# Kernel optimization log

Measured on AMD Instinct MI355X. Metric: run time of the kernel, lower is better.

The kernel has to match this reference:

```python
import jax, jax.numpy as jnp
import numpy as np

N_SRC = 100000
N_TGT = 100000
N_EDGES = 1600000
D = 128
HID = 128
OUT = 64
NUM_LAYERS = 2
P_DROP = 0.1
NEG_SLOPE = 0.01


def setup_inputs() -> dict:
    key = jax.random.key(0)
    ks = jax.random.split(key, 16)
    s = 1.0 / np.sqrt(D)
    inp = {
        "x_source": jax.random.normal(ks[0], (N_SRC, D), jnp.float32),
        "x_target": jax.random.normal(ks[1], (N_TGT, D), jnp.float32),
        "Wl_tgt": jax.random.normal(ks[2], (NUM_LAYERS, D, HID), jnp.float32) * s,
        "bl_tgt": jax.random.normal(ks[3], (NUM_LAYERS, HID), jnp.float32) * s,
        "Wr_tgt": jax.random.normal(ks[4], (NUM_LAYERS, D, HID), jnp.float32) * s,
        "Wl_src": jax.random.normal(ks[5], (NUM_LAYERS, D, HID), jnp.float32) * s,
        "bl_src": jax.random.normal(ks[6], (NUM_LAYERS, HID), jnp.float32) * s,
        "Wr_src": jax.random.normal(ks[7], (NUM_LAYERS, D, HID), jnp.float32) * s,
        "W_out": jax.random.normal(ks[8], (HID, OUT), jnp.float32) * (1.0 / np.sqrt(HID)),
        "b_out": jax.random.normal(ks[9], (OUT,), jnp.float32) * 0.01,
        "edge_src": jax.random.randint(ks[10], (N_EDGES,), 0, N_SRC, jnp.int32),
        "edge_dst": jax.random.randint(ks[11], (N_EDGES,), 0, N_TGT, jnp.int32),
        "rev_src": jax.random.randint(ks[12], (N_EDGES,), 0, N_TGT, jnp.int32),
        "rev_dst": jax.random.randint(ks[13], (N_EDGES,), 0, N_SRC, jnp.int32),
    }
    return inp


def _sage(x_src, x_dst, src_idx, dst_idx, n_dst, Wl, bl, Wr):
    # mean-aggregate neighbor messages per destination node (PyG SAGEConv default)
    msg = x_src[src_idx]  # [E, D] gather
    agg = jax.ops.segment_sum(msg, dst_idx, num_segments=n_dst)  # [n_dst, D]
    cnt = jax.ops.segment_sum(jnp.ones((src_idx.shape[0],), msg.dtype), dst_idx,
                              num_segments=n_dst)
    mean = agg / jnp.maximum(cnt, 1.0)[:, None]
    return mean @ Wl + bl + x_dst @ Wr


def _dropout(x, key):
    keep = jax.random.bernoulli(key, 1.0 - P_DROP, x.shape)
    return jnp.where(keep, x / (1.0 - P_DROP), jnp.zeros((), x.dtype))


def reference(x_source, x_target, Wl_tgt, bl_tgt, Wr_tgt, Wl_src, bl_src, Wr_src,
              W_out, b_out, edge_src, edge_dst, rev_src, rev_dst):
    dkey = jax.random.key(42)
    xs, xt = x_source, x_target
    for l in range(NUM_LAYERS):
        # ('source','edge','target'): target receives from source
        new_t = _sage(xs, xt, edge_src, edge_dst, N_TGT, Wl_tgt[l], bl_tgt[l], Wr_tgt[l])
        # ('target','rev_edge','source'): source receives from target
        new_s = _sage(xt, xs, rev_src, rev_dst, N_SRC, Wl_src[l], bl_src[l], Wr_src[l])
        new_t = jax.nn.leaky_relu(new_t, NEG_SLOPE)
        new_s = jax.nn.leaky_relu(new_s, NEG_SLOPE)
        new_t = _dropout(new_t, jax.random.fold_in(dkey, 2 * l))
        new_s = _dropout(new_s, jax.random.fold_in(dkey, 2 * l + 1))
        xs, xt = new_s, new_t
    return xs @ W_out + b_out
```

## Files before the change

### kernel.cpp

```cpp
#include <hip/hip_runtime.h>
#include <stdint.h>

#define NN 100000
#define NE 1600000
#define DD 128
#define HB 1024
#define G8 12544
#define SUBN 98
#define NSUB 128
#define NND 100352
#define K2 16
#define RCAP 2304
#define MSKB 1563

typedef unsigned short u16;
typedef unsigned long long u64;
typedef short short8 __attribute__((ext_vector_type(8)));
typedef float floatx4 __attribute__((ext_vector_type(4)));
typedef float floatx2 __attribute__((ext_vector_type(2)));
typedef int intx4 __attribute__((ext_vector_type(4)));

__device__ static inline u16 f2bf(float f){
  unsigned u = __float_as_uint(f);
  unsigned r = u + 0x7FFFu + ((u >> 16) & 1u);
  return (u16)(r >> 16);
}

__host__ __device__ static inline unsigned rotl32(unsigned x, int r){
  return (x << r) | (x >> (32 - r));
}

__host__ __device__ static inline void tf2x32(unsigned k0, unsigned k1,
                                              unsigned c0, unsigned c1,
                                              unsigned &o0, unsigned &o1)
{
  const unsigned ks2 = k0 ^ k1 ^ 0x1BD11BDAu;
  unsigned x0 = c0 + k0, x1 = c1 + k1;
#define TFR(r) { x0 += x1; x1 = rotl32(x1, (r)); x1 ^= x0; }
  TFR(13) TFR(15) TFR(26) TFR(6)   x0 += k1;  x1 += ks2 + 1u;
  TFR(17) TFR(29) TFR(16) TFR(24)  x0 += ks2; x1 += k0 + 2u;
  TFR(13) TFR(15) TFR(26) TFR(6)   x0 += k0;  x1 += k1 + 3u;
  TFR(17) TFR(29) TFR(16) TFR(24)  x0 += k1;  x1 += ks2 + 4u;
  TFR(13) TFR(15) TFR(26) TFR(6)   x0 += ks2; x1 += k0 + 5u;
#undef TFR
  o0 = x0; o1 = x1;
}

__device__ static inline int drop_keep(unsigned k0, unsigned k1, unsigned j)
{
  unsigned o0, o1;
  tf2x32(k0, k1, 0u, j, o0, o1);
  const unsigned bits = o0 ^ o1;
  const float u = __uint_as_float((bits >> 9) | 0x3F800000u) - 1.0f;
  return u < 0.9f;
}

__device__ static inline void mask_body(u64* __restrict__ mp,
                                        unsigned kk0, unsigned kk1, int mb){
  const int wave = threadIdx.x >> 6, lane = threadIdx.x & 63;
  const int base = mb * 64 + wave * 16;
  for (int i2 = 0; i2 < 16; ++i2){
    int r = base + i2;
    if (r >= NN) break;
    u64 mA = __ballot(drop_keep(kk0, kk1, (unsigned)r * 128u + (unsigned)lane));
    u64 mB = __ballot(drop_keep(kk0, kk1, (unsigned)r * 128u + 64u + (unsigned)lane));
    if (lane < 2) mp[(size_t)r * 2 + lane] = lane ? mB : mA;
  }
}

#define CVB 12500
__global__ __launch_bounds__(256) void k_pre(
    const float* __restrict__ ina, const float* __restrict__ inb,
    u16* __restrict__ oa, u16* __restrict__ ob, int n8,
    const int* __restrict__ e_dst, const int* __restrict__ r_dst,
    int* __restrict__ hist,
    const float* __restrict__ Wl_tgt, const float* __restrict__ Wr_tgt,
    const float* __restrict__ Wl_src, const float* __restrict__ Wr_src,
    const float* __restrict__ Wo,
    u16* __restrict__ Wsw0, u16* __restrict__ Wsw1, u16* __restrict__ Wsw2,
    u16* __restrict__ Wswo)
{
  const int blk = blockIdx.x;
  const int t = threadIdx.x;
  if (blk < CVB){
    int i = blk * 256 + t;
    const float* in = ina; u16* out = oa;
    if (i >= n8){ i -= n8; in = inb; out = ob; }
    floatx4 a = __builtin_nontemporal_load((const floatx4*)in + (size_t)i * 2);
    floatx4 c = __builtin_nontemporal_load((const floatx4*)in + (size_t)i * 2 + 1);
    u16 v[8] = { f2bf(a[0]), f2bf(a[1]), f2bf(a[2]), f2bf(a[3]),
                 f2bf(c[0]), f2bf(c[1]), f2bf(c[2]), f2bf(c[3]) };
    *(uint4*)(out + (size_t)i * 8) = *(const uint4*)v;
  } else if (blk < CVB + HB){
    const int hb = blk - CVB;
    __shared__ int h[16];
    if (t < 16) h[t] = 0;
    __syncthreads();
    const int QT = 2 * (NE / 4);
    for (int i = hb * 256 + t; i < QT; i += HB * 256){
      int dir = (i >= NE / 4);
      int qi = dir ? i - NE / 4 : i;
      const int* dp = dir ? r_dst : e_dst;
      intx4 d = __builtin_nontemporal_load((const intx4*)dp + qi);
      int bb = dir << 3;
      atomicAdd(&h[bb + d.x / G8], 1);
      atomicAdd(&h[bb + d.y / G8], 1);
      atomicAdd(&h[bb + d.z / G8], 1);
      atomicAdd(&h[bb + d.w / G8], 1);
    }
    __syncthreads();
    if (t < 16) hist[t * HB + hb] = h[t];
  } else {
    int b = blk - CVB - HB;
    if (b < 48){
      const float *Wl, *Wr; u16* dst;
      if (b < 16){ Wl = Wl_tgt; Wr = Wr_tgt; dst = Wsw0; }
      else if (b < 32){ Wl = Wl_src; Wr = Wr_src; dst = Wsw1; b -= 16; }
      else { Wl = Wl_src + 16384; Wr = Wr_src + 16384; dst = Wsw2; b -= 32; }
      int idx = b * 256 + t;
      int lane = idx & 63, tile = idx >> 6;
      int kt = tile >> 3, nt = tile & 7;
      int n = nt * 16 + (lane & 15);
      int kb = kt * 32 + (lane >> 4) * 8;
      u16 v[8];
      #pragma unroll
      for (int j = 0; j < 8; ++j){
        int k = kb + j;
        float w = (k < 128) ? Wl[(size_t)k * 128 + n] : Wr[(size_t)(k - 128) * 128 + n];
        v[j] = f2bf(w);
      }
      *(uint4*)(dst + (size_t)idx * 8) = *(const uint4*)v;
    } else {
      int idx = (b - 48) * 256 + t;
      int lane = idx & 63, tile = idx >> 6;
      int kt = tile >> 2, nt = tile & 3;
      int n = nt * 16 + (lane & 15);
      int kb = kt * 32 + (lane >> 4) * 8;
      u16 v[8];
      #pragma unroll
      for (int j = 0; j < 8; ++j)
        v[j] = f2bf(Wo[(size_t)(kb + j) * 64 + n]);
      *(uint4*)(Wswo + (size_t)idx * 8) = *(const uint4*)v;
    }
  }
}

__global__ __launch_bounds__(256) void k_scanA(int* __restrict__ hist){
  __shared__ int sh[16 * HB];
  __shared__ int tot[256];
  const int t = threadIdx.x;
  const int N = 16 * HB;
  for (int k = t; k < N; k += 256) sh[k] = hist[k];
  __syncthreads();
  int s = 0;
  #pragma unroll 4
  for (int k = 0; k < 64; ++k)
    s += sh[(t >> 4) * HB + (t & 15) + (k << 4)];
  tot[t] = s;
  __syncthreads();
  int v = s;
  for (int off = 1; off < 256; off <<= 1){
    int u = (t >= off) ? tot[t - off] : 0;
    __syncthreads();
    tot[t] += u;
    __syncthreads();
  }
  int run = tot[t] - v;
  for (int k = 0; k < 64; ++k){
    int idx = (t >> 4) * HB + (t & 15) + (k << 4);
    int xv = sh[idx];
    sh[idx] = run;
    run += xv;
  }
  __syncthreads();
  for (int k = t; k < N; k += 256) hist[k] = sh[k];
  if (t == 255) hist[N] = tot[255];
}

__global__ __launch_bounds__(256) void k_scatter1(const int* __restrict__ e_src,
                                                  const int* __restrict__ e_dst,
                                                  const int* __restrict__ r_src,
                                                  const int* __restrict__ r_dst,
                                                  const int* __restrict__ base,
                                                  unsigned* __restrict__ stage,
                                                  u64* __restrict__ M0t,
                                                  unsigned ka, unsigned kb){
  const int b = blockIdx.x;
  const int q = b / 5, rm = b % 5;
  if (rm >= 2){
    int mb = q * 3 + (rm - 2);
    if (mb < MSKB) mask_body(M0t, ka, kb, mb);
    return;
  }
  const int sb = q * 2 + rm;
  if (sb >= HB) return;
  __shared__ int cur[16];
  const int t = threadIdx.x;
  if (t < 16) cur[t] = base[t * HB + sb];
  __syncthreads();
  const int QT = 2 * (NE / 4);
  for (int i = sb * 256 + t; i < QT; i += HB * 256){
    int dir = (i >= NE / 4);
    int qi = dir ? i - NE / 4 : i;
    const int* dp = dir ? r_dst : e_dst;
    const int* sp = dir ? r_src : e_src;
    intx4 d = __builtin_nontemporal_load((const intx4*)dp + qi);
    intx4 sv = __builtin_nontemporal_load((const intx4*)sp + qi);
    int bb = dir << 3;
    int g, p;
    g = d.x / G8; p = atomicAdd(&cur[bb + g], 1);
    stage[p] = (unsigned)sv.x | ((unsigned)(d.x - g * G8) << 17);
    g = d.y / G8; p = atomicAdd(&cur[bb + g], 1);
    stage[p] = (unsigned)sv.y | ((unsigned)(d.y - g * G8) << 17);
    g = d.z / G8; p = atomicAdd(&cur[bb + g], 1);
    stage[p] = (unsigned)sv.z | ((unsigned)(d.z - g * G8) << 17);
    g = d.w / G8; p = atomicAdd(&cur[bb + g], 1);
    stage[p] = (unsigned)sv.w | ((unsigned)(d.w - g * G8) << 17);
  }
}

__global__ __launch_bounds__(256) void k_hist2(const unsigned* __restrict__ stage,
                                               const int* __restrict__ base,
                                               int* __restrict__ hist2){
  __shared__ int h2[NSUB];
  const int b16 = blockIdx.x / K2, k = blockIdx.x % K2;
  const int t = threadIdx.x;
  if (t < NSUB) h2[t] = 0;
  __syncthreads();
  const int beg = base[b16 * HB];
  const int end = base[(b16 + 1) * HB];
  for (int i = beg + k * 256 + t; i < end; i += K2 * 256){
    unsigned p = stage[i];
    atomicAdd(&h2[(int)(p >> 17) / SUBN], 1);
  }
  __syncthreads();
  if (t < NSUB) hist2[(b16 * NSUB + t) * K2 + k] = h2[t];
}

__global__ __launch_bounds__(256) void k_scanB(int* __restrict__ hist2){
  __shared__ int sh[16 * NSUB * K2];
  __shared__ int tot[256];
  const int t = threadIdx.x;
  const int N = 16 * NSUB * K2;
  for (int k = t; k < N; k += 256) sh[k] = hist2[k];
  __syncthreads();
  int s = 0;
  for (int j = 0; j < 128; ++j) s += sh[t * 128 + j];
  tot[t] = s;
  __syncthreads();
  int v = s;
  for (int off = 1; off < 256; off <<= 1){
    int u = (t >= off) ? tot[t - off] : 0;
    __syncthreads();
    tot[t] += u;
    __syncthreads();
  }
  int run = tot[t] - v;
  for (int j = 0; j < 128; ++j){
    int xv = sh[t * 128 + j];
    sh[t * 128 + j] = run;
    run += xv;
  }
  __syncthreads();
  for (int k = t; k < N; k += 256) hist2[k] = sh[k];
}

__global__ __launch_bounds__(256) void k_scatter2(const unsigned* __restrict__ stage,
                                                  const int* __restrict__ base,
                                                  const int* __restrict__ h2s,
                                                  unsigned* __restrict__ stage2,
                                                  u64* __restrict__ M0s,
                                                  unsigned ka, unsigned kb){
  const int b = blockIdx.x;
  const int q = b / 7, rm = b % 7;
  if (rm >= 1){
    int mb = q * 6 + (rm - 1);
    if (mb < MSKB) mask_body(M0s, ka, kb, mb);
    return;
  }
  const int sb = q;
  if (sb >= 16 * K2) return;
  __shared__ int cur[NSUB];
  const int b16 = sb / K2, k = sb % K2;
  const int t = threadIdx.x;
  if (t < NSUB) cur[t] = h2s[(b16 * NSUB + t) * K2 + k];
  __syncthreads();
  const int beg = base[b16 * HB];
  const int end = base[(b16 + 1) * HB];
  for (int i = beg + k * 256 + t; i < end; i += K2 * 256){
    unsigned p = stage[i];
    int pos = atomicAdd(&cur[(int)(p >> 17) / SUBN], 1);
    stage2[pos] = p;
  }
}

__global__ __launch_bounds__(256) void k_fill4(const unsigned* __restrict__ stage2,
                                               const int* __restrict__ h2s,
                                               int* __restrict__ ptr,
                                               int* __restrict__ csr){
  __shared__ unsigned rec[RCAP];
  __shared__ unsigned srt[RCAP];
  __shared__ int ldeg[SUBN], lptr[SUBN], lcur[SUBN];
  const int sb = blockIdx.x;
  const int b16 = sb >> 7, sub = sb & 127;
  const int dir = b16 >> 3, g = b16 & 7;
  const int t = threadIdx.x;
  const int beg = h2s[sb * K2];
  const int end = (sb == 2047) ? 2 * NE : h2s[(sb + 1) * K2];
  int n = end - beg;
  if (n > RCAP) n = RCAP;
  for (int i = t; i < n; i += 256) rec[i] = stage2[beg + i];
  if (t < SUBN) ldeg[t] = 0;
  __syncthreads();
  const int nl0 = sub * SUBN;
  for (int i = t; i < n; i += 256)
    atomicAdd(&ldeg[(int)(rec[i] >> 17) - nl0], 1);
  __syncthreads();
  if (t == 0){
    int run = 0;
    for (int s = 0; s < SUBN; ++s){ lptr[s] = run; lcur[s] = run; run += ldeg[s]; }
  }
  __syncthreads();
  for (int i = t; i < n; i += 256){
    int rl = (int)(rec[i] >> 17) - nl0;
    int pos = atomicAdd(&lcur[rl], 1);
    srt[pos] = rec[i] & 0x1FFFFu;
  }
  __syncthreads();
  const int node0 = g * G8 + nl0;
  if (t < SUBN) ptr[dir * NND + node0 + t] = beg + lptr[t];
  if (sb == 2047 && t == 0) ptr[2 * NND] = 2 * NE;
  for (int i = t; i < n; i += 256) csr[beg + i] = (int)srt[i];
}

template<bool WM>
__device__ static inline void agg_body(const u16* __restrict__ x,
                                       const int* __restrict__ pd,
                                       const int* __restrict__ csr,
                                       u16* __restrict__ out,
                                       u64* __restrict__ msk,
                                       unsigned key0, unsigned key1, int blk){
  const int row = blk * 4 + (threadIdx.x >> 6);
  const int lane = threadIdx.x & 63;
  const int sub = lane >> 4, l4 = lane & 15;
  const int beg = pd[row], end = pd[row + 1];
  const int cnt = end - beg;
  floatx2 p0 = (floatx2)0.f, p1 = (floatx2)0.f, p2 = (floatx2)0.f, p3 = (floatx2)0.f;
#define ACC4(v) { \
    floatx2 t0, t1, t2, t3; \
    t0[0] = __uint_as_float((v).x << 16); t0[1] = __uint_as_float((v).x & 0xFFFF0000u); \
    t1[0] = __uint_as_float((v).y << 16); t1[1] = __uint_as_float((v).y & 0xFFFF0000u); \
    t2[0] = __uint_as_float((v).z << 16); t2[1] = __uint_as_float((v).z & 0xFFFF0000u); \
    t3[0] = __uint_as_float((v).w << 16); t3[1] = __uint_as_float((v).w & 0xFFFF0000u); \
    p0 += t0; p1 += t1; p2 += t2; p3 += t3; }
  int e = 0;
  for (; e + 7 < cnt; e += 8){
    int s0 = csr[beg + e + sub];
    int s1 = csr[beg + e + 4 + sub];
    uint4 v0 = *(const uint4*)(x + (size_t)s0 * DD + l4 * 8);
    uint4 v1 = *(const uint4*)(x + (size_t)s1 * DD + l4 * 8);
    ACC4(v0);
    ACC4(v1);
  }
  for (; e + 3 < cnt; e += 4){
    int s0 = csr[beg + e + sub];
    uint4 v0 = *(const uint4*)(x + (size_t)s0 * DD + l4 * 8);
    ACC4(v0);
  }
  if (e + sub < cnt){
    int s0 = csr[beg + e + sub];
    uint4 v0 = *(const uint4*)(x + (size_t)s0 * DD + l4 * 8);
    ACC4(v0);
  }
#undef ACC4
  if (WM){
    u64 mA = __ballot(drop_keep(key0, key1, (unsigned)row * 128u + (unsigned)lane));
    u64 mB = __ballot(drop_keep(key0, key1, (unsigned)row * 128u + 64u + (unsigned)lane));
    if (lane < 2) msk[(size_t)row * 2 + lane] = lane ? mB : mA;
  }
  float a[8] = { p0[0], p0[1], p1[0], p1[1], p2[0], p2[1], p3[0], p3[1] };
  #pragma unroll
  for (int i = 0; i < 8; ++i){
    a[i] += __shfl_xor(a[i], 16);
    a[i] += __shfl_xor(a[i], 32);
  }
  const float inv = (cnt > 0) ? (1.0f / (float)cnt) : 1.0f;
  if (sub == 0){
    unsigned pk[4];
    #pragma unroll
    for (int i = 0; i < 4; ++i)
      pk[i] = (unsigned)f2bf(a[2*i] * inv) | ((unsigned)f2bf(a[2*i+1] * inv) << 16);
    *(uint4*)(out + (size_t)row * DD + l4 * 8) = make_uint4(pk[0], pk[1], pk[2], pk[3]);
  }
}

__global__ __launch_bounds__(256) void k_aggD(const u16* __restrict__ x0,
    const u16* __restrict__ x1, const int* __restrict__ ptr,
    const int* __restrict__ csr, u16* __restrict__ o0, u16* __restrict__ o1){
  int b = blockIdx.x;
  if (b < NN / 4) agg_body<false>(x0, ptr, csr, o0, nullptr, 0u, 0u, b);
  else            agg_body<false>(x1, ptr + NND, csr, o1, nullptr, 0u, 0u, b - NN / 4);
}

__global__ __launch_bounds__(256) void k_agg1(const u16* __restrict__ x,
    const int* __restrict__ ptr, const int* __restrict__ csr,
    u16* __restrict__ out, u64* __restrict__ msk,
    unsigned key0, unsigned key1){
  agg_body<true>(x, ptr + NND, csr, out, msk, key0, key1, blockIdx.x);
}

__device__ static inline void fused_body(const u16* __restrict__ Am,
    const u16* __restrict__ X, const u16* __restrict__ Wsw,
    const float* __restrict__ bias, u16* __restrict__ outH,
    const u64* __restrict__ msk, int blk)
{
  const int wave = threadIdx.x >> 6, lane = threadIdx.x & 63;
  const int quad = lane >> 4, col0 = lane & 15;
  const int row0 = blk * 64 + wave * 16;
  int m = row0 + col0;
  if (m >= NN) m = NN - 1;

  floatx4 acc[8];
  #pragma unroll
  for (int i = 0; i < 8; ++i) acc[i] = (floatx4)0.f;

  #pragma unroll
  for (int kt = 0; kt < 8; ++kt){
    const int k = kt * 32 + quad * 8;
    const u16* ap = (k < 128) ? (Am + (size_t)m * 128 + k)
                              : (X  + (size_t)m * 128 + (k - 128));
    short8 a = __builtin_nontemporal_load((const short8*)ap);
    #pragma unroll
    for (int nt = 0; nt < 8; ++nt){
      short8 b = *(const short8*)(Wsw + (size_t)(((kt * 8 + nt) * 64 + lane) * 8));
      acc[nt] = __builtin_amdgcn_mfma_f32_16x16x32_bf16(a, b, acc[nt], 0, 0, 0);
    }
  }

  u64 w0[4], w1[4];
  #pragma unroll
  for (int rg = 0; rg < 4; ++rg){
    int r = row0 + quad * 4 + rg;
    size_t rr = (size_t)((r < NN) ? r : (NN - 1)) * 2;
    w0[rg] = msk[rr];
    w1[rg] = msk[rr + 1];
  }

  #pragma unroll
  for (int nt = 0; nt < 8; ++nt){
    const int col = nt * 16 + col0;
    const float bj = bias[col];
    const int sh = col & 63;
    #pragma unroll
    for (int rg = 0; rg < 4; ++rg){
      const int r = row0 + quad * 4 + rg;
      if (r < NN){
        float h = acc[nt][rg] + bj;
        h = (h >= 0.f) ? h : 0.01f * h;
        u64 w = (nt < 4) ? w0[rg] : w1[rg];
        h = ((w >> sh) & 1ull) ? h * (1.0f / 0.9f) : 0.0f;
        outH[(size_t)r * 128 + col] = f2bf(h);
      }
    }
  }
}

#define GB ((NN + 63) / 64)

__global__ __launch_bounds__(256) void k_fusedD(
    const u16* __restrict__ A0, const u16* __restrict__ X0,
    const u16* __restrict__ W0, const float* __restrict__ b0,
    u16* __restrict__ o0, const u64* __restrict__ m0,
    const u16* __restrict__ A1, const u16* __restrict__ X1,
    const u16* __restrict__ W1, const float* __restrict__ b1,
    u16* __restrict__ o1, const u64* __restrict__ m1)
{
  int b = blockIdx.x;
  if (b < GB) fused_body(A0, X0, W0, b0, o0, m0, b);
  else        fused_body(A1, X1, W1, b1, o1, m1, b - GB);
}

__global__ __launch_bounds__(256) void k_fused(const u16* __restrict__ Am,
    const u16* __restrict__ X, const u16* __restrict__ Wsw,
    const float* __restrict__ bias, u16* __restrict__ outH,
    const u64* __restrict__ msk)
{
  fused_body(Am, X, Wsw, bias, outH, msk, blockIdx.x);
}

__global__ __launch_bounds__(256) void k_out(const u16* __restrict__ H,
    const u16* __restrict__ Wsw, const float* __restrict__ bias,
    float* __restrict__ out)
{
  const int wave = threadIdx.x >> 6, lane = threadIdx.x & 63;
  const int quad = lane >> 4, col0 = lane & 15;
  const int row0 = blockIdx.x * 64 + wave * 16;
  int m = row0 + col0;
  if (m >= NN) m = NN - 1;

  floatx4 acc[4];
  #pragma unroll
  for (int i = 0; i < 4; ++i) acc[i] = (floatx4)0.f;

  #pragma unroll
  for (int kt = 0; kt < 4; ++kt){
    short8 a = __builtin_nontemporal_load(
        (const short8*)(H + (size_t)m * 128 + kt * 32 + quad * 8));
    #pragma unroll
    for (int nt = 0; nt < 4; ++nt){
      short8 b = *(const short8*)(Wsw + (size_t)(((kt * 4 + nt) * 64 + lane) * 8));
      acc[nt] = __builtin_amdgcn_mfma_f32_16x16x32_bf16(a, b, acc[nt], 0, 0, 0);
    }
  }

  #pragma unroll
  for (int nt = 0; nt < 4; ++nt){
    const int col = nt * 16 + col0;
    const float bj = bias[col];
    #pragma unroll
    for (int rg = 0; rg < 4; ++rg){
      const int r = row0 + quad * 4 + rg;
      if (r < NN)
        out[(size_t)r * 64 + col] = acc[nt][rg] + bj;
    }
  }
}

extern "C" void kernel_launch(void* const* d_in, const int* in_sizes, int n_in,
                              void* d_out, int out_size, void* d_ws, size_t ws_size,
                              hipStream_t stream)
{
  const float* x_src  = (const float*)d_in[0];
  const float* x_tgt  = (const float*)d_in[1];
  const float* Wl_tgt = (const float*)d_in[2];
  const float* bl_tgt = (const float*)d_in[3];
  const float* Wr_tgt = (const float*)d_in[4];
  const float* Wl_src = (const float*)d_in[5];
  const float* bl_src = (const float*)d_in[6];
  const float* Wr_src = (const float*)d_in[7];
  const float* W_o    = (const float*)d_in[8];
  const float* b_o    = (const float*)d_in[9];
  const int*   e_src  = (const int*)d_in[10];
  const int*   e_dst  = (const int*)d_in[11];
  const int*   r_src  = (const int*)d_in[12];
  const int*   r_dst  = (const int*)d_in[13];
  float* out = (float*)d_out;
  (void)in_sizes; (void)n_in; (void)out_size; (void)ws_size;

  char* ws = (char*)d_ws;
  size_t off = 0;
  auto alloc = [&](size_t bytes) -> char* {
    char* p = ws + off; off += (bytes + 255) & ~(size_t)255; return p;
  };
  unsigned* stage1 = (unsigned*)alloc((size_t)2 * NE * 4);
  unsigned* stage2 = (unsigned*)alloc((size_t)2 * NE * 4);
  u16* A_t  = (u16*)stage1;
  u16* A_s  = (u16*)alloc((size_t)NN * DD * 2);
  u16* Xs   = (u16*)alloc((size_t)NN * DD * 2);
  u16* Xt   = (u16*)alloc((size_t)NN * DD * 2);
  u16* B    = (u16*)alloc((size_t)NN * DD * 2);
  u16* C    = (u16*)alloc((size_t)NN * DD * 2);
  u16* Wsw0 = (u16*)alloc(256 * 128 * 2);
  u16* Wsw1 = (u16*)alloc(256 * 128 * 2);
  u16* Wsw2 = (u16*)alloc(256 * 128 * 2);
  u16* Wswo = (u16*)alloc(128 * 64 * 2);
  int* csr  = (int*)alloc((size_t)2 * NE * 4);
  int* ptr  = (int*)alloc((size_t)(2 * NND + 1) * 4);
  int* hist  = (int*)alloc((size_t)(16 * HB + 1) * 4);
  int* hist2 = (int*)alloc((size_t)(16 * NSUB * K2) * 4);
  u64* M0t  = (u64*)alloc((size_t)NN * 2 * 8);
  u64* M0s  = (u64*)alloc((size_t)NN * 2 * 8);
  u64* M1s  = (u64*)alloc((size_t)NN * 2 * 8);

  unsigned kt0a, kt0b, ks0a, ks0b, ks1a, ks1b;
  tf2x32(0u, 42u, 0u, 0u, kt0a, kt0b);
  tf2x32(0u, 42u, 0u, 1u, ks0a, ks0b);
  tf2x32(0u, 42u, 0u, 3u, ks1a, ks1b);

  k_pre<<<CVB + HB + 52, 256, 0, stream>>>(x_src, x_tgt, Xs, Xt, NN * DD / 8,
                                           e_dst, r_dst, hist,
                                           Wl_tgt, Wr_tgt, Wl_src, Wr_src, W_o,
                                           Wsw0, Wsw1, Wsw2, Wswo);
  k_scanA<<<1, 256, 0, stream>>>(hist);
  k_scatter1<<<5 * 521, 256, 0, stream>>>(e_src, e_dst, r_src, r_dst, hist,
                                          stage1, M0t, kt0a, kt0b);
  k_hist2<<<16 * K2, 256, 0, stream>>>(stage1, hist, hist2);
  k_scanB<<<1, 256, 0, stream>>>(hist2);
  k_scatter2<<<7 * 261, 256, 0, stream>>>(stage1, hist, hist2, stage2,
                                          M0s, ks0a, ks0b);
  k_fill4<<<2048, 256, 0, stream>>>(stage2, hist2, ptr, csr);

  const int AB = NN / 4;
  k_aggD<<<2 * AB, 256, 0, stream>>>(Xs, Xt, ptr, csr, A_t, A_s);
  k_fusedD<<<2 * GB, 256, 0, stream>>>(A_t, Xt, Wsw0, bl_tgt, B, M0t,
                                       A_s, Xs, Wsw1, bl_src, C, M0s);
  k_agg1<<<AB, 256, 0, stream>>>(B, ptr, csr, A_t, M1s, ks1a, ks1b);
  k_fused<<<GB, 256, 0, stream>>>(A_t, C, Wsw2, bl_src + 128, B, M1s);
  k_out<<<GB, 256, 0, stream>>>(B, Wswo, b_o, out);
}
```

Before: 608.6 us.

## Sort CSR neighbors by source bucket and move dropout mask into aggregation

k_fill4 now counting-sorts each destination's edges by a composite key of local destination row and the source index's high bits, using a parallel block scan in place of a single-thread serial scan. Grouping neighbors by source range is meant to improve gather locality in the aggregation kernels. The M0t dropout-mask generation moves out of k_scatter1 and into the first half of k_aggD. This simplifies the scatter launch but adds mask work to the aggregation kernel and more shared-memory scan steps in fill.

```diff
diff --git a/kernel.cpp b/kernel.cpp
--- a/kernel.cpp
+++ b/kernel.cpp
@@ -12,6 +12,7 @@
 #define K2 16
 #define RCAP 2304
 #define MSKB 1563
+#define NKEY (SUBN * 16)
 
 typedef unsigned short u16;
 typedef unsigned long long u64;
@@ -182,24 +183,13 @@
                                                   const int* __restrict__ r_src,
                                                   const int* __restrict__ r_dst,
                                                   const int* __restrict__ base,
-                                                  unsigned* __restrict__ stage,
-                                                  u64* __restrict__ M0t,
-                                                  unsigned ka, unsigned kb){
-  const int b = blockIdx.x;
-  const int q = b / 5, rm = b % 5;
-  if (rm >= 2){
-    int mb = q * 3 + (rm - 2);
-    if (mb < MSKB) mask_body(M0t, ka, kb, mb);
-    return;
-  }
-  const int sb = q * 2 + rm;
-  if (sb >= HB) return;
+                                                  unsigned* __restrict__ stage){
   __shared__ int cur[16];
   const int t = threadIdx.x;
-  if (t < 16) cur[t] = base[t * HB + sb];
+  if (t < 16) cur[t] = base[t * HB + blockIdx.x];
   __syncthreads();
   const int QT = 2 * (NE / 4);
-  for (int i = sb * 256 + t; i < QT; i += HB * 256){
+  for (int i = blockIdx.x * 256 + t; i < QT; i += HB * 256){
     int dir = (i >= NE / 4);
     int qi = dir ? i - NE / 4 : i;
     const int* dp = dir ? r_dst : e_dst;
@@ -300,7 +290,9 @@
                                                int* __restrict__ csr){
   __shared__ unsigned rec[RCAP];
   __shared__ unsigned srt[RCAP];
-  __shared__ int ldeg[SUBN], lptr[SUBN], lcur[SUBN];
+  __shared__ int ldeg[NKEY];
+  __shared__ int lptr[NKEY];
+  __shared__ int tsum[256];
   const int sb = blockIdx.x;
   const int b16 = sb >> 7, sub = sb & 127;
   const int dir = b16 >> 3, g = b16 & 7;
@@ -310,26 +302,49 @@
   int n = end - beg;
   if (n > RCAP) n = RCAP;
   for (int i = t; i < n; i += 256) rec[i] = stage2[beg + i];
-  if (t < SUBN) ldeg[t] = 0;
+  for (int i = t; i < NKEY; i += 256) ldeg[i] = 0;
   __syncthreads();
   const int nl0 = sub * SUBN;
-  for (int i = t; i < n; i += 256)
-    atomicAdd(&ldeg[(int)(rec[i] >> 17) - nl0], 1);
-  __syncthreads();
-  if (t == 0){
-    int run = 0;
-    for (int s = 0; s < SUBN; ++s){ lptr[s] = run; lcur[s] = run; run += ldeg[s]; }
-  }
-  __syncthreads();
   for (int i = t; i < n; i += 256){
-    int rl = (int)(rec[i] >> 17) - nl0;
-    int pos = atomicAdd(&lcur[rl], 1);
-    srt[pos] = rec[i] & 0x1FFFFu;
+    unsigned r = rec[i];
+    int key = (((int)(r >> 17) - nl0) << 4) | (int)((r & 0x1FFFFu) >> 13);
+    atomicAdd(&ldeg[key], 1);
+  }
+  __syncthreads();
+  int myloc[7]; int s = 0;
+  #pragma unroll
+  for (int j = 0; j < 7; ++j){
+    int idx = t * 7 + j;
+    int v = (idx < NKEY) ? ldeg[idx] : 0;
+    myloc[j] = s; s += v;
+  }
+  tsum[t] = s;
+  __syncthreads();
+  int v0 = s;
+  for (int off = 1; off < 256; off <<= 1){
+    int u = (t >= off) ? tsum[t - off] : 0;
+    __syncthreads();
+    tsum[t] += u;
+    __syncthreads();
+  }
+  int run = tsum[t] - v0;
+  #pragma unroll
+  for (int j = 0; j < 7; ++j){
+    int idx = t * 7 + j;
+    if (idx < NKEY) lptr[idx] = run + myloc[j];
   }
   __syncthreads();
   const int node0 = g * G8 + nl0;
-  if (t < SUBN) ptr[dir * NND + node0 + t] = beg + lptr[t];
+  if (t < SUBN) ptr[dir * NND + node0 + t] = beg + lptr[t * 16];
   if (sb == 2047 && t == 0) ptr[2 * NND] = 2 * NE;
+  __syncthreads();
+  for (int i = t; i < n; i += 256){
+    unsigned r = rec[i];
+    int key = (((int)(r >> 17) - nl0) << 4) | (int)((r & 0x1FFFFu) >> 13);
+    int pos = atomicAdd(&lptr[key], 1);
+    srt[pos] = r & 0x1FFFFu;
+  }
+  __syncthreads();
   for (int i = t; i < n; i += 256) csr[beg + i] = (int)srt[i];
 }
 
@@ -396,9 +411,10 @@
 
 __global__ __launch_bounds__(256) void k_aggD(const u16* __restrict__ x0,
     const u16* __restrict__ x1, const int* __restrict__ ptr,
-    const int* __restrict__ csr, u16* __restrict__ o0, u16* __restrict__ o1){
+    const int* __restrict__ csr, u16* __restrict__ o0, u16* __restrict__ o1,
+    u64* __restrict__ m0, unsigned k00, unsigned k01){
   int b = blockIdx.x;
-  if (b < NN / 4) agg_body<false>(x0, ptr, csr, o0, nullptr, 0u, 0u, b);
+  if (b < NN / 4) agg_body<true>(x0, ptr, csr, o0, m0, k00, k01, b);
   else            agg_body<false>(x1, ptr + NND, csr, o1, nullptr, 0u, 0u, b - NN / 4);
 }
 
@@ -582,8 +598,7 @@
                                            Wl_tgt, Wr_tgt, Wl_src, Wr_src, W_o,
                                            Wsw0, Wsw1, Wsw2, Wswo);
   k_scanA<<<1, 256, 0, stream>>>(hist);
-  k_scatter1<<<5 * 521, 256, 0, stream>>>(e_src, e_dst, r_src, r_dst, hist,
-                                          stage1, M0t, kt0a, kt0b);
+  k_scatter1<<<HB, 256, 0, stream>>>(e_src, e_dst, r_src, r_dst, hist, stage1);
   k_hist2<<<16 * K2, 256, 0, stream>>>(stage1, hist, hist2);
   k_scanB<<<1, 256, 0, stream>>>(hist2);
   k_scatter2<<<7 * 261, 256, 0, stream>>>(stage1, hist, hist2, stage2,
@@ -591,7 +606,8 @@
   k_fill4<<<2048, 256, 0, stream>>>(stage2, hist2, ptr, csr);
 
   const int AB = NN / 4;
-  k_aggD<<<2 * AB, 256, 0, stream>>>(Xs, Xt, ptr, csr, A_t, A_s);
+  k_aggD<<<2 * AB, 256, 0, stream>>>(Xs, Xt, ptr, csr, A_t, A_s,
+                                     M0t, kt0a, kt0b);
   k_fusedD<<<2 * GB, 256, 0, stream>>>(A_t, Xt, Wsw0, bl_tgt, B, M0t,
                                        A_s, Xs, Wsw1, bl_src, C, M0s);
   k_agg1<<<AB, 256, 0, stream>>>(B, ptr, csr, A_t, M1s, ks1a, ks1b);
```

After: 585.8 us. 3.7% less time.

## Replace two-pass edge sort with single-pass 2048-bin counting sort

Applied to the files above, without the earlier changes.

Replaces the two-level radix partition (coarse histogram, scan, scatter, sub-histogram, scan, scatter) with one fine-grained 2048-bin histogram reduced into global atomics, a single small scan, and a one-pass scatter. The scatter uses per-block shared-memory counts and reserves space with global atomics. Dropout mask generation moves from the scatter kernels into the first aggregation kernel. The aggregation loop also gets a 16-edge unrolled step. This removes several kernel launches and one full pass over the staged edges, at the cost of heavier shared-memory atomics and more contended global atomics.

```diff
diff --git a/kernel.cpp b/kernel.cpp
--- a/kernel.cpp
+++ b/kernel.cpp
@@ -4,14 +4,13 @@
 #define NN 100000
 #define NE 1600000
 #define DD 128
-#define HB 1024
 #define G8 12544
 #define SUBN 98
-#define NSUB 128
 #define NND 100352
-#define K2 16
 #define RCAP 2304
-#define MSKB 1563
+#define NBIN 2048
+#define HBH 256
+#define SB2 512
 
 typedef unsigned short u16;
 typedef unsigned long long u64;
@@ -55,17 +54,20 @@
   return u < 0.9f;
 }
 
-__device__ static inline void mask_body(u64* __restrict__ mp,
-                                        unsigned kk0, unsigned kk1, int mb){
-  const int wave = threadIdx.x >> 6, lane = threadIdx.x & 63;
-  const int base = mb * 64 + wave * 16;
-  for (int i2 = 0; i2 < 16; ++i2){
-    int r = base + i2;
-    if (r >= NN) break;
-    u64 mA = __ballot(drop_keep(kk0, kk1, (unsigned)r * 128u + (unsigned)lane));
-    u64 mB = __ballot(drop_keep(kk0, kk1, (unsigned)r * 128u + 64u + (unsigned)lane));
-    if (lane < 2) mp[(size_t)r * 2 + lane] = lane ? mB : mA;
-  }
+__device__ static inline void acc4(floatx2 &p0, floatx2 &p1, floatx2 &p2,
+                                   floatx2 &p3, uint4 v){
+  floatx2 t0, t1, t2, t3;
+  t0[0] = __uint_as_float(v.x << 16); t0[1] = __uint_as_float(v.x & 0xFFFF0000u);
+  t1[0] = __uint_as_float(v.y << 16); t1[1] = __uint_as_float(v.y & 0xFFFF0000u);
+  t2[0] = __uint_as_float(v.z << 16); t2[1] = __uint_as_float(v.z & 0xFFFF0000u);
+  t3[0] = __uint_as_float(v.w << 16); t3[1] = __uint_as_float(v.w & 0xFFFF0000u);
+  p0 += t0; p1 += t1; p2 += t2; p3 += t3;
+}
+
+__device__ static inline int dbin(int dir, int d, int &nl){
+  int g = d / G8;
+  nl = d - g * G8;
+  return (dir << 10) | (g << 7) | (nl / SUBN);
 }
 
 #define CVB 12500
@@ -73,7 +75,7 @@
     const float* __restrict__ ina, const float* __restrict__ inb,
     u16* __restrict__ oa, u16* __restrict__ ob, int n8,
     const int* __restrict__ e_dst, const int* __restrict__ r_dst,
-    int* __restrict__ hist,
+    int* __restrict__ histg,
     const float* __restrict__ Wl_tgt, const float* __restrict__ Wr_tgt,
     const float* __restrict__ Wl_src, const float* __restrict__ Wr_src,
     const float* __restrict__ Wo,
@@ -91,27 +93,30 @@
     u16 v[8] = { f2bf(a[0]), f2bf(a[1]), f2bf(a[2]), f2bf(a[3]),
                  f2bf(c[0]), f2bf(c[1]), f2bf(c[2]), f2bf(c[3]) };
     *(uint4*)(out + (size_t)i * 8) = *(const uint4*)v;
-  } else if (blk < CVB + HB){
+  } else if (blk < CVB + HBH){
     const int hb = blk - CVB;
-    __shared__ int h[16];
-    if (t < 16) h[t] = 0;
+    __shared__ int h2[NBIN];
+    for (int i = t; i < NBIN; i += 256) h2[i] = 0;
     __syncthreads();
     const int QT = 2 * (NE / 4);
-    for (int i = hb * 256 + t; i < QT; i += HB * 256){
+    for (int i = hb * 256 + t; i < QT; i += HBH * 256){
       int dir = (i >= NE / 4);
       int qi = dir ? i - NE / 4 : i;
       const int* dp = dir ? r_dst : e_dst;
       intx4 d = __builtin_nontemporal_load((const intx4*)dp + qi);
-      int bb = dir << 3;
-      atomicAdd(&h[bb + d.x / G8], 1);
-      atomicAdd(&h[bb + d.y / G8], 1);
-      atomicAdd(&h[bb + d.z / G8], 1);
-      atomicAdd(&h[bb + d.w / G8], 1);
+      int nl;
+      atomicAdd(&h2[dbin(dir, d.x, nl)], 1);
+      atomicAdd(&h2[dbin(dir, d.y, nl)], 1);
+      atomicAdd(&h2[dbin(dir, d.z, nl)], 1);
+      atomicAdd(&h2[dbin(dir, d.w, nl)], 1);
     }
     __syncthreads();
-    if (t < 16) hist[t * HB + hb] = h[t];
+    for (int i = t; i < NBIN; i += 256){
+      int c = h2[i];
+      if (c) atomicAdd(&histg[i], c);
+    }
   } else {
-    int b = blk - CVB - HB;
+    int b = blk - CVB - HBH;
     if (b < 48){
       const float *Wl, *Wr; u16* dst;
       if (b < 16){ Wl = Wl_tgt; Wr = Wr_tgt; dst = Wsw0; }
@@ -145,157 +150,89 @@
   }
 }
 
-__global__ __launch_bounds__(256) void k_scanA(int* __restrict__ hist){
-  __shared__ int sh[16 * HB];
+__global__ __launch_bounds__(256) void k_scan2(const int* __restrict__ histg,
+                                               int* __restrict__ base2,
+                                               int* __restrict__ gcur){
   __shared__ int tot[256];
   const int t = threadIdx.x;
-  const int N = 16 * HB;
-  for (int k = t; k < N; k += 256) sh[k] = hist[k];
-  __syncthreads();
-  int s = 0;
-  #pragma unroll 4
-  for (int k = 0; k < 64; ++k)
-    s += sh[(t >> 4) * HB + (t & 15) + (k << 4)];
+  int v[8]; int s = 0;
+  #pragma unroll
+  for (int j = 0; j < 8; ++j){ v[j] = s; s += histg[t * 8 + j]; }
   tot[t] = s;
   __syncthreads();
-  int v = s;
+  int mine = s;
   for (int off = 1; off < 256; off <<= 1){
     int u = (t >= off) ? tot[t - off] : 0;
     __syncthreads();
     tot[t] += u;
     __syncthreads();
   }
-  int run = tot[t] - v;
-  for (int k = 0; k < 64; ++k){
-    int idx = (t >> 4) * HB + (t & 15) + (k << 4);
-    int xv = sh[idx];
-    sh[idx] = run;
-    run += xv;
-  }
-  __syncthreads();
-  for (int k = t; k < N; k += 256) hist[k] = sh[k];
-  if (t == 255) hist[N] = tot[255];
-}
-
-__global__ __launch_bounds__(256) void k_scatter1(const int* __restrict__ e_src,
-                                                  const int* __restrict__ e_dst,
-                                                  const int* __restrict__ r_src,
-                                                  const int* __restrict__ r_dst,
-                                                  const int* __restrict__ base,
-                                                  unsigned* __restrict__ stage,
-                                                  u64* __restrict__ M0t,
-                                                  unsigned ka, unsigned kb){
-  const int b = blockIdx.x;
-  const int q = b / 5, rm = b % 5;
-  if (rm >= 2){
-    int mb = q * 3 + (rm - 2);
-    if (mb < MSKB) mask_body(M0t, ka, kb, mb);
-    return;
-  }
-  const int sb = q * 2 + rm;
-  if (sb >= HB) return;
-  __shared__ int cur[16];
+  int run = tot[t] - mine;
+  #pragma unroll
+  for (int j = 0; j < 8; ++j){
+    base2[t * 8 + j] = run + v[j];
+    gcur[t * 8 + j]  = run + v[j];
+  }
+  if (t == 0) base2[NBIN] = 2 * NE;
+}
+
+__global__ __launch_bounds__(256) void k_scat(const int* __restrict__ e_src,
+                                              const int* __restrict__ e_dst,
+                                              const int* __restrict__ r_src,
+                                              const int* __restrict__ r_dst,
+                                              int* __restrict__ gcur,
+                                              unsigned* __restrict__ stage){
+  __shared__ intx4 dq[7 * 256];
+  __shared__ int lcnt[NBIN], lbase[NBIN], lcur[NBIN];
   const int t = threadIdx.x;
-  if (t < 16) cur[t] = base[t * HB + sb];
-  __syncthreads();
   const int QT = 2 * (NE / 4);
-  for (int i = sb * 256 + t; i < QT; i += HB * 256){
-    int dir = (i >= NE / 4);
-    int qi = dir ? i - NE / 4 : i;
-    const int* dp = dir ? r_dst : e_dst;
-    const int* sp = dir ? r_src : e_src;
-    intx4 d = __builtin_nontemporal_load((const intx4*)dp + qi);
-    intx4 sv = __builtin_nontemporal_load((const intx4*)sp + qi);
-    int bb = dir << 3;
-    int g, p;
-    g = d.x / G8; p = atomicAdd(&cur[bb + g], 1);
-    stage[p] = (unsigned)sv.x | ((unsigned)(d.x - g * G8) << 17);
-    g = d.y / G8; p = atomicAdd(&cur[bb + g], 1);
-    stage[p] = (unsigned)sv.y | ((unsigned)(d.y - g * G8) << 17);
-    g = d.z / G8; p = atomicAdd(&cur[bb + g], 1);
-    stage[p] = (unsigned)sv.z | ((unsigned)(d.z - g * G8) << 17);
-    g = d.w / G8; p = atomicAdd(&cur[bb + g], 1);
-    stage[p] = (unsigned)sv.w | ((unsigned)(d.w - g * G8) << 17);
-  }
-}
-
-__global__ __launch_bounds__(256) void k_hist2(const unsigned* __restrict__ stage,
-                                               const int* __restrict__ base,
-                                               int* __restrict__ hist2){
-  __shared__ int h2[NSUB];
-  const int b16 = blockIdx.x / K2, k = blockIdx.x % K2;
-  const int t = threadIdx.x;
-  if (t < NSUB) h2[t] = 0;
-  __syncthreads();
-  const int beg = base[b16 * HB];
-  const int end = base[(b16 + 1) * HB];
-  for (int i = beg + k * 256 + t; i < end; i += K2 * 256){
-    unsigned p = stage[i];
-    atomicAdd(&h2[(int)(p >> 17) / SUBN], 1);
-  }
-  __syncthreads();
-  if (t < NSUB) hist2[(b16 * NSUB + t) * K2 + k] = h2[t];
-}
-
-__global__ __launch_bounds__(256) void k_scanB(int* __restrict__ hist2){
-  __shared__ int sh[16 * NSUB * K2];
-  __shared__ int tot[256];
-  const int t = threadIdx.x;
-  const int N = 16 * NSUB * K2;
-  for (int k = t; k < N; k += 256) sh[k] = hist2[k];
-  __syncthreads();
-  int s = 0;
-  for (int j = 0; j < 128; ++j) s += sh[t * 128 + j];
-  tot[t] = s;
-  __syncthreads();
-  int v = s;
-  for (int off = 1; off < 256; off <<= 1){
-    int u = (t >= off) ? tot[t - off] : 0;
-    __syncthreads();
-    tot[t] += u;
-    __syncthreads();
-  }
-  int run = tot[t] - v;
-  for (int j = 0; j < 128; ++j){
-    int xv = sh[t * 128 + j];
-    sh[t * 128 + j] = run;
-    run += xv;
-  }
-  __syncthreads();
-  for (int k = t; k < N; k += 256) hist2[k] = sh[k];
-}
-
-__global__ __launch_bounds__(256) void k_scatter2(const unsigned* __restrict__ stage,
-                                                  const int* __restrict__ base,
-                                                  const int* __restrict__ h2s,
-                                                  unsigned* __restrict__ stage2,
-                                                  u64* __restrict__ M0s,
-                                                  unsigned ka, unsigned kb){
-  const int b = blockIdx.x;
-  const int q = b / 7, rm = b % 7;
-  if (rm >= 1){
-    int mb = q * 6 + (rm - 1);
-    if (mb < MSKB) mask_body(M0s, ka, kb, mb);
-    return;
-  }
-  const int sb = q;
-  if (sb >= 16 * K2) return;
-  __shared__ int cur[NSUB];
-  const int b16 = sb / K2, k = sb % K2;
-  const int t = threadIdx.x;
-  if (t < NSUB) cur[t] = h2s[(b16 * NSUB + t) * K2 + k];
-  __syncthreads();
-  const int beg = base[b16 * HB];
-  const int end = base[(b16 + 1) * HB];
-  for (int i = beg + k * 256 + t; i < end; i += K2 * 256){
-    unsigned p = stage[i];
-    int pos = atomicAdd(&cur[(int)(p >> 17) / SUBN], 1);
-    stage2[pos] = p;
-  }
-}
-
-__global__ __launch_bounds__(256) void k_fill4(const unsigned* __restrict__ stage2,
-                                               const int* __restrict__ h2s,
+  for (int i = t; i < NBIN; i += 256) lcnt[i] = 0;
+  __syncthreads();
+  {
+    int j = 0;
+    for (int i = blockIdx.x * 256 + t; i < QT; i += SB2 * 256, ++j){
+      int dir = (i >= NE / 4);
+      int qi = dir ? i - NE / 4 : i;
+      const int* dp = dir ? r_dst : e_dst;
+      intx4 d = __builtin_nontemporal_load((const intx4*)dp + qi);
+      dq[j * 256 + t] = d;
+      int nl;
+      atomicAdd(&lcnt[dbin(dir, d.x, nl)], 1);
+      atomicAdd(&lcnt[dbin(dir, d.y, nl)], 1);
+      atomicAdd(&lcnt[dbin(dir, d.z, nl)], 1);
+      atomicAdd(&lcnt[dbin(dir, d.w, nl)], 1);
+    }
+  }
+  __syncthreads();
+  for (int i = t; i < NBIN; i += 256){
+    int c = lcnt[i];
+    lbase[i] = c ? atomicAdd(&gcur[i], c) : 0;
+    lcur[i] = 0;
+  }
+  __syncthreads();
+  {
+    int j = 0;
+    for (int i = blockIdx.x * 256 + t; i < QT; i += SB2 * 256, ++j){
+      int dir = (i >= NE / 4);
+      int qi = dir ? i - NE / 4 : i;
+      const int* sp = dir ? r_src : e_src;
+      intx4 s = __builtin_nontemporal_load((const intx4*)sp + qi);
+      intx4 d = dq[j * 256 + t];
+      int nl, b, p;
+      b = dbin(dir, d.x, nl); p = lbase[b] + atomicAdd(&lcur[b], 1);
+      stage[p] = (unsigned)s.x | ((unsigned)nl << 17);
+      b = dbin(dir, d.y, nl); p = lbase[b] + atomicAdd(&lcur[b], 1);
+      stage[p] = (unsigned)s.y | ((unsigned)nl << 17);
+      b = dbin(dir, d.z, nl); p = lbase[b] + atomicAdd(&lcur[b], 1);
+      stage[p] = (unsigned)s.z | ((unsigned)nl << 17);
+      b = dbin(dir, d.w, nl); p = lbase[b] + atomicAdd(&lcur[b], 1);
+      stage[p] = (unsigned)s.w | ((unsigned)nl << 17);
+    }
+  }
+}
+
+__global__ __launch_bounds__(256) void k_fill4(const unsigned* __restrict__ stage,
+                                               const int* __restrict__ base2,
                                                int* __restrict__ ptr,
                                                int* __restrict__ csr){
   __shared__ unsigned rec[RCAP];
@@ -305,11 +242,11 @@
   const int b16 = sb >> 7, sub = sb & 127;
   const int dir = b16 >> 3, g = b16 & 7;
   const int t = threadIdx.x;
-  const int beg = h2s[sb * K2];
-  const int end = (sb == 2047) ? 2 * NE : h2s[(sb + 1) * K2];
+  const int beg = base2[sb];
+  const int end = base2[sb + 1];
   int n = end - beg;
   if (n > RCAP) n = RCAP;
-  for (int i = t; i < n; i += 256) rec[i] = stage2[beg + i];
+  for (int i = t; i < n; i += 256) rec[i] = stage[beg + i];
   if (t < SUBN) ldeg[t] = 0;
   __syncthreads();
   const int nl0 = sub * SUBN;
@@ -346,33 +283,39 @@
   const int beg = pd[row], end = pd[row + 1];
   const int cnt = end - beg;
   floatx2 p0 = (floatx2)0.f, p1 = (floatx2)0.f, p2 = (floatx2)0.f, p3 = (floatx2)0.f;
-#define ACC4(v) { \
-    floatx2 t0, t1, t2, t3; \
-    t0[0] = __uint_as_float((v).x << 16); t0[1] = __uint_as_float((v).x & 0xFFFF0000u); \
-    t1[0] = __uint_as_float((v).y << 16); t1[1] = __uint_as_float((v).y & 0xFFFF0000u); \
-    t2[0] = __uint_as_float((v).z << 16); t2[1] = __uint_as_float((v).z & 0xFFFF0000u); \
-    t3[0] = __uint_as_float((v).w << 16); t3[1] = __uint_as_float((v).w & 0xFFFF0000u); \
-    p0 += t0; p1 += t1; p2 += t2; p3 += t3; }
   int e = 0;
+  for (; e + 15 < cnt; e += 16){
+    int s0 = csr[beg + e + sub];
+    int s1 = csr[beg + e + 4 + sub];
+    int s2 = csr[beg + e + 8 + sub];
+    int s3 = csr[beg + e + 12 + sub];
+    uint4 v0 = *(const uint4*)(x + (size_t)s0 * DD + l4 * 8);
+    uint4 v1 = *(const uint4*)(x + (size_t)s1 * DD + l4 * 8);
+    uint4 v2 = *(const uint4*)(x + (size_t)s2 * DD + l4 * 8);
+    uint4 v3 = *(const uint4*)(x + (size_t)s3 * DD + l4 * 8);
+    acc4(p0, p1, p2, p3, v0);
+    acc4(p0, p1, p2, p3, v1);
+    acc4(p0, p1, p2, p3, v2);
+    acc4(p0, p1, p2, p3, v3);
+  }
   for (; e + 7 < cnt; e += 8){
     int s0 = csr[beg + e + sub];
     int s1 = csr[beg + e + 4 + sub];
     uint4 v0 = *(const uint4*)(x + (size_t)s0 * DD + l4 * 8);
     uint4 v1 = *(const uint4*)(x + (size_t)s1 * DD + l4 * 8);
-    ACC4(v0);
-    ACC4(v1);
+    acc4(p0, p1, p2, p3, v0);
+    acc4(p0, p1, p2, p3, v1);
   }
   for (; e + 3 < cnt; e += 4){
     int s0 = csr[beg + e + sub];
     uint4 v0 = *(const uint4*)(x + (size_t)s0 * DD + l4 * 8);
-    ACC4(v0);
+    acc4(p0, p1, p2, p3, v0);
   }
   if (e + sub < cnt){
     int s0 = csr[beg + e + sub];
     uint4 v0 = *(const uint4*)(x + (size_t)s0 * DD + l4 * 8);
-    ACC4(v0);
-  }
-#undef ACC4
+    acc4(p0, p1, p2, p3, v0);
+  }
   if (WM){
     u64 mA = __ballot(drop_keep(key0, key1, (unsigned)row * 128u + (unsigned)lane));
     u64 mB = __ballot(drop_keep(key0, key1, (unsigned)row * 128u + 64u + (unsigned)lane));
@@ -396,10 +339,12 @@
 
 __global__ __launch_bounds__(256) void k_aggD(const u16* __restrict__ x0,
     const u16* __restrict__ x1, const int* __restrict__ ptr,
-    const int* __restrict__ csr, u16* __restrict__ o0, u16* __restrict__ o1){
+    const int* __restrict__ csr, u16* __restrict__ o0, u16* __restrict__ o1,
+    u64* __restrict__ m0, u64* __restrict__ m1,
+    unsigned k00, unsigned k01, unsigned k10, unsigned k11){
   int b = blockIdx.x;
-  if (b < NN / 4) agg_body<false>(x0, ptr, csr, o0, nullptr, 0u, 0u, b);
-  else            agg_body<false>(x1, ptr + NND, csr, o1, nullptr, 0u, 0u, b - NN / 4);
+  if (b < NN / 4) agg_body<true>(x0, ptr, csr, o0, m0, k00, k01, b);
+  else            agg_body<true>(x1, ptr + NND, csr, o1, m1, k10, k11, b - NN / 4);
 }
 
 __global__ __launch_bounds__(256) void k_agg1(const u16* __restrict__ x,
@@ -552,9 +497,8 @@
   auto alloc = [&](size_t bytes) -> char* {
     char* p = ws + off; off += (bytes + 255) & ~(size_t)255; return p;
   };
-  unsigned* stage1 = (unsigned*)alloc((size_t)2 * NE * 4);
-  unsigned* stage2 = (unsigned*)alloc((size_t)2 * NE * 4);
-  u16* A_t  = (u16*)stage1;
+  unsigned* stage = (unsigned*)alloc((size_t)2 * NE * 8);
+  u16* A_t  = (u16*)stage;
   u16* A_s  = (u16*)alloc((size_t)NN * DD * 2);
   u16* Xs   = (u16*)alloc((size_t)NN * DD * 2);
   u16* Xt   = (u16*)alloc((size_t)NN * DD * 2);
@@ -566,8 +510,9 @@
   u16* Wswo = (u16*)alloc(128 * 64 * 2);
   int* csr  = (int*)alloc((size_t)2 * NE * 4);
   int* ptr  = (int*)alloc((size_t)(2 * NND + 1) * 4);
-  int* hist  = (int*)alloc((size_t)(16 * HB + 1) * 4);
-  int* hist2 = (int*)alloc((size_t)(16 * NSUB * K2) * 4);
+  int* histg = (int*)alloc((size_t)NBIN * 4);
+  int* base2 = (int*)alloc((size_t)(NBIN + 1) * 4);
+  int* gcur  = (int*)alloc((size_t)NBIN * 4);
   u64* M0t  = (u64*)alloc((size_t)NN * 2 * 8);
   u64* M0s  = (u64*)alloc((size_t)NN * 2 * 8);
   u64* M1s  = (u64*)alloc((size_t)NN * 2 * 8);
@@ -577,21 +522,18 @@
   tf2x32(0u, 42u, 0u, 1u, ks0a, ks0b);
   tf2x32(0u, 42u, 0u, 3u, ks1a, ks1b);
 
-  k_pre<<<CVB + HB + 52, 256, 0, stream>>>(x_src, x_tgt, Xs, Xt, NN * DD / 8,
-                                           e_dst, r_dst, hist,
-                                           Wl_tgt, Wr_tgt, Wl_src, Wr_src, W_o,
-                                           Wsw0, Wsw1, Wsw2, Wswo);
-  k_scanA<<<1, 256, 0, stream>>>(hist);
-  k_scatter1<<<5 * 521, 256, 0, stream>>>(e_src, e_dst, r_src, r_dst, hist,
-                                          stage1, M0t, kt0a, kt0b);
-  k_hist2<<<16 * K2, 256, 0, stream>>>(stage1, hist, hist2);
-  k_scanB<<<1, 256, 0, stream>>>(hist2);
-  k_scatter2<<<7 * 261, 256, 0, stream>>>(stage1, hist, hist2, stage2,
-                                          M0s, ks0a, ks0b);
-  k_fill4<<<2048, 256, 0, stream>>>(stage2, hist2, ptr, csr);
+  hipMemsetAsync(histg, 0, (size_t)NBIN * 4, stream);
+  k_pre<<<CVB + HBH + 52, 256, 0, stream>>>(x_src, x_tgt, Xs, Xt, NN * DD / 8,
+                                            e_dst, r_dst, histg,
+                                            Wl_tgt, Wr_tgt, Wl_src, Wr_src, W_o,
+                                            Wsw0, Wsw1, Wsw2, Wswo);
+  k_scan2<<<1, 256, 0, stream>>>(histg, base2, gcur);
+  k_scat<<<SB2, 256, 0, stream>>>(e_src, e_dst, r_src, r_dst, gcur, stage);
+  k_fill4<<<2048, 256, 0, stream>>>(stage, base2, ptr, csr);
 
   const int AB = NN / 4;
-  k_aggD<<<2 * AB, 256, 0, stream>>>(Xs, Xt, ptr, csr, A_t, A_s);
+  k_aggD<<<2 * AB, 256, 0, stream>>>(Xs, Xt, ptr, csr, A_t, A_s,
+                                     M0t, M0s, kt0a, kt0b, ks0a, ks0b);
   k_fusedD<<<2 * GB, 256, 0, stream>>>(A_t, Xt, Wsw0, bl_tgt, B, M0t,
                                        A_s, Xs, Wsw1, bl_src, C, M0s);
   k_agg1<<<AB, 256, 0, stream>>>(B, ptr, csr, A_t, M1s, ks1a, ks1b);
```

Result: faster. 550.9 us (-9.5%).
